# Kernel tuning notes

Hardware: AMD Instinct MI355X
Metric: run time of the kernel (lower is better)

The kernel has to match this reference:

```python
import jax, jax.numpy as jnp
import numpy as np

V = 25   # NTU joints
NE = 5   # number of hyper-edge types


def setup_inputs() -> dict:
    key = jax.random.key(0)
    ks = jax.random.split(key, 8)
    N, C, T = 64, 12, 300
    x = jax.random.normal(ks[0], (N, C, T, V), dtype=jnp.float32)
    # binary incidence matrices [V, E] with E == V, as in the NTU hyper-edge tables
    hs = [jax.random.bernoulli(ks[1 + i], 0.2, (V, V)).astype(jnp.float32) for i in range(NE)]
    in_ch, out_ch = 3, 64
    w_mlp = jax.random.normal(ks[6], (out_ch, in_ch * NE), dtype=jnp.float32) * (1.0 / np.sqrt(in_ch * NE))
    b_mlp = jnp.zeros((out_ch,), dtype=jnp.float32)
    return {"x": x, "h_local": hs[0], "h_center": hs[1], "h_figl": hs[2],
            "h_figr": hs[3], "h_hand": hs[4], "w_mlp": w_mlp, "b_mlp": b_mlp}


def _normalized_aggregate(w, h):
    # w: [N, T, E], h: [V, E] (E == V)
    degree_v = jnp.einsum('ve,bte->btv', h, w)
    # pow(d, -0.5): inf at d==0 and nan at d<0 are both zeroed in the original
    dv_pos = degree_v > 0
    degree_v = jnp.where(dv_pos, jax.lax.rsqrt(jnp.where(dv_pos, degree_v, 1.0)), 0.0)
    degree_e = jnp.sum(h, axis=0)                      # [E]
    de_nz = degree_e != 0
    degree_e = jnp.where(de_nz, 1.0 / jnp.where(de_nz, degree_e, 1.0), 0.0)
    # fused dh * w * degree_e chain: [N, T, V, E]
    dhwb = degree_v[..., None] * h[None, None] * w[:, :, None, :] * degree_e
    dhwbht = jnp.einsum('btve,ue->btvu', dhwb, h)      # [N, T, V, V]
    return dhwbht * degree_v[:, :, None, :]


def reference(x, h_local, h_center, h_figl, h_figr, h_hand, w_mlp, b_mlp):
    ws = (x[:, 6], x[:, 7], x[:, 9], x[:, 10], x[:, 11])
    hs = (h_local, h_center, h_figl, h_figr, h_hand)
    hwh_cat = jnp.concatenate([_normalized_aggregate(w, h) for w, h in zip(ws, hs)], axis=-2)  # [N,T,5V,V]
    feat = x[:, :3]                                    # [N, 3, T, V]
    N, C, T, Vv = feat.shape
    support = jnp.einsum('btvu,bctu->bctv', hwh_cat, feat)          # [N, C, T, 5V]
    support = support.reshape(N, C, T, NE, Vv).transpose(0, 3, 1, 2, 4).reshape(N, NE * C, T, Vv)
    out = jnp.einsum('oi,bitv->botv', w_mlp, support) + b_mlp[None, :, None, None]
    return jax.nn.relu(out)
```

## Files before the change

kernel.cpp:

```cpp
#include <hip/hip_runtime.h>

#define NE  5
#define V   25
#define NT  300
#define NC  12
#define CO  64
#define WPB 4
#define GX  38

typedef float f4 __attribute__((ext_vector_type(4)));
typedef float f2 __attribute__((ext_vector_type(2)));

#define WSYNC() do { asm volatile("s_waitcnt lgkmcnt(0)" ::: "memory"); \
                     __builtin_amdgcn_sched_barrier(0); } while (0)

__device__ __forceinline__ float hsel(unsigned m, int e, float w) {
    int s = ((int)(m << (31 - e))) >> 31;
    return __int_as_float(__float_as_int(w) & s);
}

#define ODV  0
#define OFP  280
#define OWB  1120
#define OBB  1568
#define OST  1408
#define SCRF 2408

__global__ __launch_bounds__(256, 4) void hyper_main(
    const float* __restrict__ x,
    const float* __restrict__ h0, const float* __restrict__ h1,
    const float* __restrict__ h2, const float* __restrict__ h3,
    const float* __restrict__ h4,
    const float* __restrict__ wmlp, const float* __restrict__ bmlp,
    float* __restrict__ out)
{
    __shared__ unsigned RM[125];
    __shared__ unsigned CM[125];
    __shared__ float    DE[125];
    __shared__ __align__(16) float SCR[WPB][SCRF];

    const int tid  = threadIdx.x;
    const int lane = tid & 63;
    const int wid  = tid >> 6;
    const int b    = blockIdx.y;

    if (tid < 125) {
        int i = tid / 25, v = tid % 25;
        const float* hp = (i==0)?h0:(i==1)?h1:(i==2)?h2:(i==3)?h3:h4;
        unsigned m = 0;
        for (int e = 0; e < V; ++e) if (hp[v*V + e] != 0.f) m |= (1u << e);
        RM[tid] = m;
    } else if (tid < 250) {
        int idx = tid - 125, i = idx / 25, e = idx % 25;
        const float* hp = (i==0)?h0:(i==1)?h1:(i==2)?h2:(i==3)?h3:h4;
        unsigned m = 0; float s = 0.f;
        for (int u = 0; u < V; ++u) {
            float hv = hp[u*V + e];
            s += hv;
            if (hv != 0.f) m |= (1u << u);
        }
        CM[idx] = m;
        DE[idx] = (s != 0.f) ? __fdiv_rn(1.f, s) : 0.f;
    }
    __syncthreads();

    const int pp = blockIdx.x * WPB + wid;
    if (pp >= NT/2) return;

    float* S = SCR[wid];

    float pf[7]; int lo[7];
    #pragma unroll
    for (int r = 0; r < 7; ++r) {
        int q  = r*64 + lane;
        int qq = (q < 400) ? q : 0;
        int tt = qq / 200, rr = qq % 200, ch = rr / 25, e = rr % 25;
        int xc = (ch < 5) ? (ch + 6 + (ch >= 2 ? 1 : 0)) : (ch - 5);
        lo[r] = OWB + tt*224 + ch*28 + e;
        pf[r] = x[((size_t)(b*NC + xc)*NT + (2*pp + tt))*V + e];
    }
    #pragma unroll
    for (int r = 0; r < 6; ++r) S[lo[r]] = pf[r];
    if (lane < 16) S[lo[6]] = pf[6];
    WSYNC();

    #pragma unroll
    for (int r = 0; r < 4; ++r) {
        int idx = r*64 + lane;
        if (idx < 250) {
            int tt  = (idx >= 125) ? 1 : 0;
            int rem = idx - (tt ? 125 : 0);
            int i = rem / 25, v = rem % 25;
            unsigned m = RM[rem];
            const float* wi = S + OWB + tt*224 + i*28;
            f4 w0 = *(const f4*)(wi+0),  w1 = *(const f4*)(wi+4),
               w2 = *(const f4*)(wi+8),  w3 = *(const f4*)(wi+12),
               w4 = *(const f4*)(wi+16), w5 = *(const f4*)(wi+20),
               w6 = *(const f4*)(wi+24);
            float L0 = 0.f, L1 = 0.f, L2 = 0.f, L3 = 0.f;
            L0=__fadd_rn(L0,hsel(m, 0,w0.x)); L1=__fadd_rn(L1,hsel(m, 1,w0.y));
            L2=__fadd_rn(L2,hsel(m, 2,w0.z)); L3=__fadd_rn(L3,hsel(m, 3,w0.w));
            L0=__fadd_rn(L0,hsel(m, 4,w1.x)); L1=__fadd_rn(L1,hsel(m, 5,w1.y));
            L2=__fadd_rn(L2,hsel(m, 6,w1.z)); L3=__fadd_rn(L3,hsel(m, 7,w1.w));
            L0=__fadd_rn(L0,hsel(m, 8,w2.x)); L1=__fadd_rn(L1,hsel(m, 9,w2.y));
            L2=__fadd_rn(L2,hsel(m,10,w2.z)); L3=__fadd_rn(L3,hsel(m,11,w2.w));
            L0=__fadd_rn(L0,hsel(m,12,w3.x)); L1=__fadd_rn(L1,hsel(m,13,w3.y));
            L2=__fadd_rn(L2,hsel(m,14,w3.z)); L3=__fadd_rn(L3,hsel(m,15,w3.w));
            L0=__fadd_rn(L0,hsel(m,16,w4.x)); L1=__fadd_rn(L1,hsel(m,17,w4.y));
            L2=__fadd_rn(L2,hsel(m,18,w4.z)); L3=__fadd_rn(L3,hsel(m,19,w4.w));
            L0=__fadd_rn(L0,hsel(m,20,w5.x)); L1=__fadd_rn(L1,hsel(m,21,w5.y));
            L2=__fadd_rn(L2,hsel(m,22,w5.z)); L3=__fadd_rn(L3,hsel(m,23,w5.w));
            float s = __fadd_rn(__fadd_rn(L0,L1), __fadd_rn(L2,L3));
            s = __fadd_rn(s, hsel(m, 24, w6.x));
            float dvv = (s > 0.f) ? (float)(1.0 / sqrt((double)s)) : 0.f;
            S[ODV + tt*140 + i*28 + v] = dvv;
            float f0  = S[OWB + tt*224 + 5*28 + v];
            float f1  = S[OWB + tt*224 + 6*28 + v];
            float f2v = S[OWB + tt*224 + 7*28 + v];
            S[OBB + tt*420 + (0*5+i)*28 + v] = dvv * f0;
            S[OBB + tt*420 + (1*5+i)*28 + v] = dvv * f1;
            S[OBB + tt*420 + (2*5+i)*28 + v] = dvv * f2v;
        }
    }
    WSYNC();

    #pragma unroll
    for (int r = 0; r < 4; ++r) {
        int idx = r*64 + lane;
        if (idx < 250) {
            int tt  = (idx >= 125) ? 1 : 0;
            int rem = idx - (tt ? 125 : 0);
            int i = rem / 25, e = rem % 25;
            unsigned m = CM[rem];
            const float* bp = S + OBB + tt*420 + i*28;
            float a0 = 0.f, a1 = 0.f, a2 = 0.f;
            while (m) {
                int u = __builtin_ctz(m); m &= m - 1;
                a0 += bp[u]; a1 += bp[140 + u]; a2 += bp[280 + u];
            }
            float gg = S[OWB + tt*224 + i*28 + e] * DE[rem];
            S[OFP + tt*420 + (i*3+0)*28 + e] = a0 * gg;
            S[OFP + tt*420 + (i*3+1)*28 + e] = a1 * gg;
            S[OFP + tt*420 + (i*3+2)*28 + e] = a2 * gg;
        }
    }
    WSYNC();

    #pragma unroll
    for (int r = 0; r < 4; ++r) {
        int idx = r*64 + lane;
        if (idx < 250) {
            int tt  = (idx >= 125) ? 1 : 0;
            int rem = idx - (tt ? 125 : 0);
            int i = rem / 25, v = rem % 25;
            unsigned m = RM[rem];
            const float* fp = S + OFP + tt*420 + i*3*28;
            float a0 = 0.f, a1 = 0.f, a2 = 0.f;
            while (m) {
                int e = __builtin_ctz(m); m &= m - 1;
                a0 += fp[e]; a1 += fp[28 + e]; a2 += fp[56 + e];
            }
            float dd = S[ODV + tt*140 + i*28 + v];
            float* st = S + OST + (tt*25 + v)*20 + i*3;
            st[0] = a0 * dd; st[1] = a1 * dd; st[2] = a2 * dd;
        }
    }
    WSYNC();

    if (lane < 50) {
        const float* st = S + OST + lane*20;
        f4 s0 = *(const f4*)(st+0), s1 = *(const f4*)(st+4),
           s2 = *(const f4*)(st+8), s3 = *(const f4*)(st+12);
        s3.w = 0.f;
        float* ob = out + (size_t)b*CO*7500 + (size_t)pp*50 + lane;
        #pragma unroll 2
        for (int o2 = 0; o2 < 32; ++o2) {
            int o = 2*o2;
            const float* wa = wmlp + o*15;
            const float* wb = wa + 15;
            f2 a = (f2){bmlp[o], bmlp[o+1]};
            a += (f2){wa[ 0], wb[ 0]} * s0.x;
            a += (f2){wa[ 1], wb[ 1]} * s0.y;
            a += (f2){wa[ 2], wb[ 2]} * s0.z;
            a += (f2){wa[ 3], wb[ 3]} * s0.w;
            a += (f2){wa[ 4], wb[ 4]} * s1.x;
            a += (f2){wa[ 5], wb[ 5]} * s1.y;
            a += (f2){wa[ 6], wb[ 6]} * s1.z;
            a += (f2){wa[ 7], wb[ 7]} * s1.w;
            a += (f2){wa[ 8], wb[ 8]} * s2.x;
            a += (f2){wa[ 9], wb[ 9]} * s2.y;
            a += (f2){wa[10], wb[10]} * s2.z;
            a += (f2){wa[11], wb[11]} * s2.w;
            a += (f2){wa[12], wb[12]} * s3.x;
            a += (f2){wa[13], wb[13]} * s3.y;
            a += (f2){wa[14], wb[14]} * s3.z;
            __builtin_nontemporal_store(fmaxf(a.x, 0.f), ob + (size_t)o*7500);
            __builtin_nontemporal_store(fmaxf(a.y, 0.f), ob + (size_t)(o+1)*7500);
        }
    }
}

extern "C" void kernel_launch(void* const* d_in, const int* in_sizes, int n_in,
                              void* d_out, int out_size, void* d_ws, size_t ws_size,
                              hipStream_t stream) {
    const float* x    = (const float*)d_in[0];
    const float* h0   = (const float*)d_in[1];
    const float* h1   = (const float*)d_in[2];
    const float* h2   = (const float*)d_in[3];
    const float* h3   = (const float*)d_in[4];
    const float* h4   = (const float*)d_in[5];
    const float* wmlp = (const float*)d_in[6];
    const float* bmlp = (const float*)d_in[7];
    float* out = (float*)d_out;

    hyper_main<<<dim3(GX, 64, 1), dim3(256,1,1), 0, stream>>>(
        x, h0, h1, h2, h3, h4, wmlp, bmlp, out);
}
```

Before: 76.11 us.

## Stage MLP weights in LDS, compact scratch layout, sparse degree sum

Each block now preloads the MLP weights and biases into a shared array, interleaved so that each output pair reads contiguous vectors from LDS. This replaces the per-iteration global or scalar loads in the output loop. The per-wave scratch layout is repacked from a 28-stride to a 25-stride, which lowers LDS footprint per block. The vertex-degree sum now walks only the set bits of the mask instead of a fully unrolled masked sum, trading fixed work for data-dependent loops that may diverge across lanes.

```diff
diff --git a/kernel.cpp b/kernel.cpp
--- a/kernel.cpp
+++ b/kernel.cpp
@@ -20,11 +20,12 @@
 }
 
 #define ODV  0
-#define OFP  280
-#define OWB  1120
-#define OBB  1568
-#define OST  1408
-#define SCRF 2408
+#define OFP  250
+#define OE_  1000
+#define OFT  1250
+#define OB_  1400
+#define OST  1000
+#define SCRF 2152
 
 __global__ __launch_bounds__(256, 4) void hyper_main(
     const float* __restrict__ x,
@@ -37,6 +38,7 @@
     __shared__ unsigned RM[125];
     __shared__ unsigned CM[125];
     __shared__ float    DE[125];
+    __shared__ __align__(16) float WPs[32*32];
     __shared__ __align__(16) float SCR[WPB][SCRF];
 
     const int tid  = threadIdx.x;
@@ -62,6 +64,11 @@
         CM[idx] = m;
         DE[idx] = (s != 0.f) ? __fdiv_rn(1.f, s) : 0.f;
     }
+    for (int q = tid; q < 1024; q += 256) {
+        int o2 = q >> 5, j = q & 31;
+        WPs[q] = (j < 30) ? wmlp[(2*o2 + (j & 1))*15 + (j >> 1)]
+                          : bmlp[2*o2 + (j - 30)];
+    }
     __syncthreads();
 
     const int pp = blockIdx.x * WPB + wid;
@@ -76,7 +83,7 @@
         int qq = (q < 400) ? q : 0;
         int tt = qq / 200, rr = qq % 200, ch = rr / 25, e = rr % 25;
         int xc = (ch < 5) ? (ch + 6 + (ch >= 2 ? 1 : 0)) : (ch - 5);
-        lo[r] = OWB + tt*224 + ch*28 + e;
+        lo[r] = ((ch < 5) ? (OE_ + tt*125 + ch*25) : (OFT + tt*75 + (ch-5)*25)) + e;
         pf[r] = x[((size_t)(b*NC + xc)*NT + (2*pp + tt))*V + e];
     }
     #pragma unroll
@@ -92,34 +99,27 @@
             int rem = idx - (tt ? 125 : 0);
             int i = rem / 25, v = rem % 25;
             unsigned m = RM[rem];
-            const float* wi = S + OWB + tt*224 + i*28;
-            f4 w0 = *(const f4*)(wi+0),  w1 = *(const f4*)(wi+4),
-               w2 = *(const f4*)(wi+8),  w3 = *(const f4*)(wi+12),
-               w4 = *(const f4*)(wi+16), w5 = *(const f4*)(wi+20),
-               w6 = *(const f4*)(wi+24);
+            const float* wi = S + OE_ + tt*125 + i*25;
             float L0 = 0.f, L1 = 0.f, L2 = 0.f, L3 = 0.f;
-            L0=__fadd_rn(L0,hsel(m, 0,w0.x)); L1=__fadd_rn(L1,hsel(m, 1,w0.y));
-            L2=__fadd_rn(L2,hsel(m, 2,w0.z)); L3=__fadd_rn(L3,hsel(m, 3,w0.w));
-            L0=__fadd_rn(L0,hsel(m, 4,w1.x)); L1=__fadd_rn(L1,hsel(m, 5,w1.y));
-            L2=__fadd_rn(L2,hsel(m, 6,w1.z)); L3=__fadd_rn(L3,hsel(m, 7,w1.w));
-            L0=__fadd_rn(L0,hsel(m, 8,w2.x)); L1=__fadd_rn(L1,hsel(m, 9,w2.y));
-            L2=__fadd_rn(L2,hsel(m,10,w2.z)); L3=__fadd_rn(L3,hsel(m,11,w2.w));
-            L0=__fadd_rn(L0,hsel(m,12,w3.x)); L1=__fadd_rn(L1,hsel(m,13,w3.y));
-            L2=__fadd_rn(L2,hsel(m,14,w3.z)); L3=__fadd_rn(L3,hsel(m,15,w3.w));
-            L0=__fadd_rn(L0,hsel(m,16,w4.x)); L1=__fadd_rn(L1,hsel(m,17,w4.y));
-            L2=__fadd_rn(L2,hsel(m,18,w4.z)); L3=__fadd_rn(L3,hsel(m,19,w4.w));
-            L0=__fadd_rn(L0,hsel(m,20,w5.x)); L1=__fadd_rn(L1,hsel(m,21,w5.y));
-            L2=__fadd_rn(L2,hsel(m,22,w5.z)); L3=__fadd_rn(L3,hsel(m,23,w5.w));
-            float s = __fadd_rn(__fadd_rn(L0,L1), __fadd_rn(L2,L3));
-            s = __fadd_rn(s, hsel(m, 24, w6.x));
+            unsigned mm;
+            mm = m & 0x00111111u;
+            while (mm) { int e = __builtin_ctz(mm); mm &= mm-1; L0 = __fadd_rn(L0, wi[e]); }
+            mm = m & 0x00222222u;
+            while (mm) { int e = __builtin_ctz(mm); mm &= mm-1; L1 = __fadd_rn(L1, wi[e]); }
+            mm = m & 0x00444444u;
+            while (mm) { int e = __builtin_ctz(mm); mm &= mm-1; L2 = __fadd_rn(L2, wi[e]); }
+            mm = m & 0x00888888u;
+            while (mm) { int e = __builtin_ctz(mm); mm &= mm-1; L3 = __fadd_rn(L3, wi[e]); }
+            float s = __fadd_rn(__fadd_rn(L0, L1), __fadd_rn(L2, L3));
+            s = __fadd_rn(s, hsel(m, 24, wi[24]));
             float dvv = (s > 0.f) ? (float)(1.0 / sqrt((double)s)) : 0.f;
-            S[ODV + tt*140 + i*28 + v] = dvv;
-            float f0  = S[OWB + tt*224 + 5*28 + v];
-            float f1  = S[OWB + tt*224 + 6*28 + v];
-            float f2v = S[OWB + tt*224 + 7*28 + v];
-            S[OBB + tt*420 + (0*5+i)*28 + v] = dvv * f0;
-            S[OBB + tt*420 + (1*5+i)*28 + v] = dvv * f1;
-            S[OBB + tt*420 + (2*5+i)*28 + v] = dvv * f2v;
+            S[ODV + tt*125 + i*25 + v] = dvv;
+            float f0  = S[OFT + tt*75 +  0 + v];
+            float f1  = S[OFT + tt*75 + 25 + v];
+            float f2v = S[OFT + tt*75 + 50 + v];
+            S[OB_ + tt*375 +   0 + i*25 + v] = dvv * f0;
+            S[OB_ + tt*375 + 125 + i*25 + v] = dvv * f1;
+            S[OB_ + tt*375 + 250 + i*25 + v] = dvv * f2v;
         }
     }
     WSYNC();
@@ -132,16 +132,16 @@
             int rem = idx - (tt ? 125 : 0);
             int i = rem / 25, e = rem % 25;
             unsigned m = CM[rem];
-            const float* bp = S + OBB + tt*420 + i*28;
+            const float* bp = S + OB_ + tt*375 + i*25;
             float a0 = 0.f, a1 = 0.f, a2 = 0.f;
             while (m) {
                 int u = __builtin_ctz(m); m &= m - 1;
-                a0 += bp[u]; a1 += bp[140 + u]; a2 += bp[280 + u];
+                a0 += bp[u]; a1 += bp[125 + u]; a2 += bp[250 + u];
             }
-            float gg = S[OWB + tt*224 + i*28 + e] * DE[rem];
-            S[OFP + tt*420 + (i*3+0)*28 + e] = a0 * gg;
-            S[OFP + tt*420 + (i*3+1)*28 + e] = a1 * gg;
-            S[OFP + tt*420 + (i*3+2)*28 + e] = a2 * gg;
+            float gg = S[OE_ + tt*125 + i*25 + e] * DE[rem];
+            S[OFP + tt*375 + (i*3+0)*25 + e] = a0 * gg;
+            S[OFP + tt*375 + (i*3+1)*25 + e] = a1 * gg;
+            S[OFP + tt*375 + (i*3+2)*25 + e] = a2 * gg;
         }
     }
     WSYNC();
@@ -154,13 +154,13 @@
             int rem = idx - (tt ? 125 : 0);
             int i = rem / 25, v = rem % 25;
             unsigned m = RM[rem];
-            const float* fp = S + OFP + tt*420 + i*3*28;
+            const float* fp = S + OFP + tt*375 + i*3*25;
             float a0 = 0.f, a1 = 0.f, a2 = 0.f;
             while (m) {
                 int e = __builtin_ctz(m); m &= m - 1;
-                a0 += fp[e]; a1 += fp[28 + e]; a2 += fp[56 + e];
+                a0 += fp[e]; a1 += fp[25 + e]; a2 += fp[50 + e];
             }
-            float dd = S[ODV + tt*140 + i*28 + v];
+            float dd = S[ODV + tt*125 + i*25 + v];
             float* st = S + OST + (tt*25 + v)*20 + i*3;
             st[0] = a0 * dd; st[1] = a1 * dd; st[2] = a2 * dd;
         }
@@ -175,27 +175,29 @@
         float* ob = out + (size_t)b*CO*7500 + (size_t)pp*50 + lane;
         #pragma unroll 2
         for (int o2 = 0; o2 < 32; ++o2) {
-            int o = 2*o2;
-            const float* wa = wmlp + o*15;
-            const float* wb = wa + 15;
-            f2 a = (f2){bmlp[o], bmlp[o+1]};
-            a += (f2){wa[ 0], wb[ 0]} * s0.x;
-            a += (f2){wa[ 1], wb[ 1]} * s0.y;
-            a += (f2){wa[ 2], wb[ 2]} * s0.z;
-            a += (f2){wa[ 3], wb[ 3]} * s0.w;
-            a += (f2){wa[ 4], wb[ 4]} * s1.x;
-            a += (f2){wa[ 5], wb[ 5]} * s1.y;
-            a += (f2){wa[ 6], wb[ 6]} * s1.z;
-            a += (f2){wa[ 7], wb[ 7]} * s1.w;
-            a += (f2){wa[ 8], wb[ 8]} * s2.x;
-            a += (f2){wa[ 9], wb[ 9]} * s2.y;
-            a += (f2){wa[10], wb[10]} * s2.z;
-            a += (f2){wa[11], wb[11]} * s2.w;
-            a += (f2){wa[12], wb[12]} * s3.x;
-            a += (f2){wa[13], wb[13]} * s3.y;
-            a += (f2){wa[14], wb[14]} * s3.z;
-            __builtin_nontemporal_store(fmaxf(a.x, 0.f), ob + (size_t)o*7500);
-            __builtin_nontemporal_store(fmaxf(a.y, 0.f), ob + (size_t)(o+1)*7500);
+            const float* wp = WPs + o2*32;
+            f4 c0 = *(const f4*)(wp+ 0), c1 = *(const f4*)(wp+ 4),
+               c2 = *(const f4*)(wp+ 8), c3 = *(const f4*)(wp+12),
+               c4 = *(const f4*)(wp+16), c5 = *(const f4*)(wp+20),
+               c6 = *(const f4*)(wp+24), c7 = *(const f4*)(wp+28);
+            f2 a = (f2){c7.z, c7.w};
+            a += (f2){c0.x, c0.y} * s0.x;
+            a += (f2){c0.z, c0.w} * s0.y;
+            a += (f2){c1.x, c1.y} * s0.z;
+            a += (f2){c1.z, c1.w} * s0.w;
+            a += (f2){c2.x, c2.y} * s1.x;
+            a += (f2){c2.z, c2.w} * s1.y;
+            a += (f2){c3.x, c3.y} * s1.z;
+            a += (f2){c3.z, c3.w} * s1.w;
+            a += (f2){c4.x, c4.y} * s2.x;
+            a += (f2){c4.z, c4.w} * s2.y;
+            a += (f2){c5.x, c5.y} * s2.z;
+            a += (f2){c5.z, c5.w} * s2.w;
+            a += (f2){c6.x, c6.y} * s3.x;
+            a += (f2){c6.z, c6.w} * s3.y;
+            a += (f2){c7.x, c7.y} * s3.z;
+            __builtin_nontemporal_store(fmaxf(a.x, 0.f), ob + (size_t)(2*o2  )*7500);
+            __builtin_nontemporal_store(fmaxf(a.y, 0.f), ob + (size_t)(2*o2+1)*7500);
         }
     }
 }
```

Result: slower. 81.56 us (+7.2%).
